# Kernel optimization log

Measured on AMD Instinct MI355X. Metric: run time of the kernel, lower is better.

## Reference

```python
import jax, jax.numpy as jnp
import numpy as np

EMBED = 384
HEAD = 64


def setup_inputs() -> dict:
    key = jax.random.key(0)
    kx, kq, kk, kv = jax.random.split(key, 4)
    B, T = 4, 4096
    x = jax.random.normal(kx, (B, T, EMBED), dtype=jnp.float32)
    # torch Linear(384, 64, bias=False): weight (64, 384), y = x @ W.T.
    # Store pre-transposed as (EMBED, HEAD) so y = x @ W.
    s = 1.0 / np.sqrt(EMBED)  # kaiming-uniform-ish scale
    Wq = jax.random.uniform(kq, (EMBED, HEAD), jnp.float32, -s, s)
    Wk = jax.random.uniform(kk, (EMBED, HEAD), jnp.float32, -s, s)
    Wv = jax.random.uniform(kv, (EMBED, HEAD), jnp.float32, -s, s)
    return {"x": x, "Wq": Wq, "Wk": Wk, "Wv": Wv}


def reference(x, Wq, Wk, Wv):
    # q, k, v: [B, T, H]
    q = x @ Wq
    k = x @ Wk
    v = x @ Wv
    scale = k.shape[-1] ** (-0.5)
    scores = jnp.einsum("bth,bsh->bts", q, k) * scale  # [B, T, T]
    # Faithful to the original: tril, then mask anything equal to 0 with -inf
    # (this also masks exact zeros inside the causal region).
    tril = jnp.tril(scores)
    masked = jnp.where(tril == 0, -jnp.inf, tril)
    attn = jax.nn.softmax(masked, axis=-1)
    out = jnp.einsum("bts,bsh->bth", attn, v)  # [B, T, H]
    return out
```

## Files before the change

### kernel.cpp

```cpp
#include <hip/hip_runtime.h>
#include <hip/hip_bf16.h>
#include <stdint.h>


#define EMBED 384
#define HEAD  64
#define NB    4
#define NT    4096
#define NROWS (NB * NT)

#define SCALE_Q 0.18033688011112042f

typedef short bf16x8 __attribute__((ext_vector_type(8)));
typedef float f32x4  __attribute__((ext_vector_type(4)));

__device__ __forceinline__ unsigned short bfround(float f) {
    union { float f; unsigned u; } v; v.f = f;
    return (unsigned short)((v.u + 0x8000u) >> 16);
}
__device__ __forceinline__ unsigned packbf(float lo, float hi) {
    union { float f; unsigned u; } a, b; a.f = lo; b.f = hi;
    return ((a.u + 0x8000u) >> 16) | ((b.u + 0x8000u) & 0xFFFF0000u);
}

__global__ __launch_bounds__(256)
void wprep_kernel(const float* __restrict__ Wq,
                  const float* __restrict__ Wk,
                  const float* __restrict__ Wv,
                  unsigned short* __restrict__ Wt)
{
    int idx = blockIdx.x * 256 + threadIdx.x;
    int k = idx / 192;
    int n = idx - k * 192;
    int sel = n >> 6, nc = n & 63;
    const float* wp = (sel == 0) ? Wq : ((sel == 1) ? Wk : Wv);
    Wt[n * EMBED + k] = bfround(wp[(size_t)k * HEAD + nc]);
}

__global__ __launch_bounds__(256)
void proj_kernel(const float* __restrict__ x,
                 const unsigned short* __restrict__ Wt,
                 unsigned short* __restrict__ Qo,
                 unsigned short* __restrict__ Ko,
                 unsigned short* __restrict__ Vto)
{
    __shared__ __attribute__((aligned(16))) unsigned short ws[96][200];
    __shared__ __attribute__((aligned(16))) unsigned short xs[64][200];
    unsigned short (*vbuf)[72] = (unsigned short (*)[72])&xs[0][0];

    const int t    = threadIdx.x;
    const int w    = t >> 6;
    const int lane = t & 63;
    const int quad = lane >> 4;
    const int l16  = lane & 15;
    const int half = blockIdx.x & 1;
    const int r0   = (blockIdx.x >> 1) * 64;
    const int colbase = half * 96;

    f32x4 acc[6];
#pragma unroll
    for (int i = 0; i < 6; ++i) acc[i] = (f32x4){0.f, 0.f, 0.f, 0.f};

#pragma unroll
    for (int ph = 0; ph < 2; ++ph) {
        if (ph) __syncthreads();
        const int k0 = ph * 192;
#pragma unroll
        for (int i = 0; i < 9; ++i) {
            int idx = t + i * 256;
            int row = idx / 24, c = idx - row * 24;
            *(uint4*)&ws[row][c * 8] =
                *(const uint4*)(Wt + (size_t)(colbase + row) * EMBED + k0 + c * 8);
        }
#pragma unroll
        for (int i = 0; i < 12; ++i) {
            int idx = t + i * 256;
            int row = idx / 48, c4 = idx - row * 48;
            const float4 v = *(const float4*)(x + (size_t)(r0 + row) * EMBED + k0 + c4 * 4);
            uint2 pw; pw.x = packbf(v.x, v.y); pw.y = packbf(v.z, v.w);
            *(uint2*)&xs[row][c4 * 4] = pw;
        }
        __syncthreads();
#pragma unroll
        for (int step = 0; step < 6; ++step) {
            bf16x8 a = *(const bf16x8*)&xs[w * 16 + l16][step * 32 + quad * 8];
#pragma unroll
            for (int ng = 0; ng < 6; ++ng) {
                bf16x8 b = *(const bf16x8*)&ws[ng * 16 + l16][step * 32 + quad * 8];
                acc[ng] = __builtin_amdgcn_mfma_f32_16x16x32_bf16(a, b, acc[ng], 0, 0, 0);
            }
        }
    }
    __syncthreads();

#pragma unroll
    for (int ng = 0; ng < 6; ++ng) {
        int cg = colbase + ng * 16 + l16;
#pragma unroll
        for (int r = 0; r < 4; ++r) {
            int row = r0 + w * 16 + quad * 4 + r;
            float vv = acc[ng][r];
            if (cg < 64) {
                Qo[(size_t)row * HEAD + cg] = bfround(vv * SCALE_Q);
            } else if (cg < 128) {
                Ko[(size_t)row * HEAD + (cg - 64)] = bfround(vv);
            } else {
                vbuf[cg - 128][w * 16 + quad * 4 + r] = bfround(vv);
            }
        }
    }
    __syncthreads();
    if (half == 1) {
        const int batch = r0 >> 12;
        const int s0 = r0 & (NT - 1);
#pragma unroll
        for (int i = 0; i < 2; ++i) {
            int idx = t + i * 256;
            int d = idx >> 3, c = idx & 7;
            *(uint4*)(Vto + ((size_t)(batch * HEAD + d)) * NT + s0 + c * 8) =
                *(const uint4*)&vbuf[d][c * 8];
        }
    }
}

__global__ __launch_bounds__(256)
void attn_kernel(const unsigned short* __restrict__ Qi,
                 const unsigned short* __restrict__ Ki,
                 const unsigned short* __restrict__ Vti,
                 float* __restrict__ opart,
                 float* __restrict__ lpart)
{
    __shared__ __attribute__((aligned(16))) unsigned short Kt[64][64];
    __shared__ __attribute__((aligned(16))) unsigned short Vs[64][64];
    __shared__ __attribute__((aligned(16))) unsigned short Ps[4][16][72];

    const int t    = threadIdx.x;
    const int w    = t >> 6;
    const int lane = t & 63;
    const int quad = lane >> 4;
    const int l16  = lane & 15;

    const int u = blockIdx.x;
    int m, sp, batch;
    if (u < 256) { m = 63 - (u >> 2); sp = 0; batch = u & 3; }
    else         { int v = u - 256; m = v >> 2; sp = 1; batch = v & 3; }
    const int ntiles = (m >= sp) ? (((m - sp) >> 1) + 1) : 0;
    const int q0 = m * 64 + w * 16;

    const unsigned short* Kbg = Ki  + (size_t)batch * NT * HEAD;
    const unsigned short* Vbg = Vti + (size_t)batch * HEAD * NT;

    bf16x8 bq0, bq1;
    {
        const unsigned short* qp = Qi + (size_t)(batch * NT + q0 + l16) * HEAD + quad * 8;
        bq0 = *(const bf16x8*)(qp);
        bq1 = *(const bf16x8*)(qp + 32);
    }

    f32x4 o[4];
#pragma unroll
    for (int i = 0; i < 4; ++i) o[i] = (f32x4){0.f, 0.f, 0.f, 0.f};
    float rs = 0.f;

    const int srow0 = t >> 3, sc = t & 7;
    const int srow1 = (t + 256) >> 3;
    const int scc0 = sc ^ (srow0 & 7);
    const int scc1 = sc ^ (srow1 & 7);

    for (int j = 0; j < ntiles; ++j) {
        const int kt = sp + 2 * j;
        uint4 kr0 = *(const uint4*)(Kbg + (size_t)(kt * 64 + srow0) * HEAD + sc * 8);
        uint4 kr1 = *(const uint4*)(Kbg + (size_t)(kt * 64 + srow1) * HEAD + sc * 8);
        uint4 vr0 = *(const uint4*)(Vbg + (size_t)srow0 * NT + kt * 64 + sc * 8);
        uint4 vr1 = *(const uint4*)(Vbg + (size_t)srow1 * NT + kt * 64 + sc * 8);
        __syncthreads();
        *(uint4*)&Kt[srow0][scc0 * 8] = kr0;
        *(uint4*)&Kt[srow1][scc1 * 8] = kr1;
        *(uint4*)&Vs[srow0][scc0 * 8] = vr0;
        *(uint4*)&Vs[srow1][scc1 * 8] = vr1;
        __syncthreads();

        const int sw = l16 & 7;
        const bool diag = (kt == m);
#pragma unroll
        for (int ts = 0; ts < 4; ++ts) {
            bf16x8 ak0 = *(const bf16x8*)&Kt[ts * 16 + l16][(quad ^ sw) * 8];
            bf16x8 ak1 = *(const bf16x8*)&Kt[ts * 16 + l16][((4 + quad) ^ sw) * 8];
            f32x4 z = (f32x4){0.f, 0.f, 0.f, 0.f};
            z = __builtin_amdgcn_mfma_f32_16x16x32_bf16(ak0, bq0, z, 0, 0, 0);
            z = __builtin_amdgcn_mfma_f32_16x16x32_bf16(ak1, bq1, z, 0, 0, 0);
            float p[4];
#pragma unroll
            for (int r = 0; r < 4; ++r) {
                float pv = __builtin_amdgcn_exp2f(z[r]);
                if (diag) {
                    int sg = kt * 64 + ts * 16 + quad * 4 + r;
                    pv = (sg > q0 + l16) ? 0.f : pv;
                }
                p[r] = pv;
            }
            rs += (p[0] + p[1]) + (p[2] + p[3]);
            uint2 pw; pw.x = packbf(p[0], p[1]); pw.y = packbf(p[2], p[3]);
            *(uint2*)&Ps[w][l16][ts * 16 + quad * 4] = pw;
        }
        bf16x8 ap0 = *(const bf16x8*)&Ps[w][l16][quad * 8];
        bf16x8 ap1 = *(const bf16x8*)&Ps[w][l16][32 + quad * 8];
#pragma unroll
        for (int nd = 0; nd < 4; ++nd) {
            bf16x8 av0 = *(const bf16x8*)&Vs[nd * 16 + l16][(quad ^ sw) * 8];
            bf16x8 av1 = *(const bf16x8*)&Vs[nd * 16 + l16][((4 + quad) ^ sw) * 8];
            o[nd] = __builtin_amdgcn_mfma_f32_16x16x32_bf16(ap0, av0, o[nd], 0, 0, 0);
            o[nd] = __builtin_amdgcn_mfma_f32_16x16x32_bf16(ap1, av1, o[nd], 0, 0, 0);
        }
    }

    rs += __shfl_xor(rs, 16, 64);
    rs += __shfl_xor(rs, 32, 64);
    if (quad == 0)
        lpart[(size_t)sp * NROWS + batch * NT + q0 + l16] = rs;
    float* ob = opart + (size_t)sp * NROWS * HEAD;
#pragma unroll
    for (int r = 0; r < 4; ++r) {
        size_t off = (size_t)(batch * NT + q0 + quad * 4 + r) * HEAD;
#pragma unroll
        for (int nd = 0; nd < 4; ++nd)
            ob[off + nd * 16 + l16] = o[nd][r];
    }
}

__global__ __launch_bounds__(256)
void combine_kernel(const float* __restrict__ opart,
                    const float* __restrict__ lpart,
                    float* __restrict__ out)
{
    int gid = blockIdx.x * 256 + threadIdx.x;
    int row = gid >> 4;
    int d4  = (gid & 15) * 4;
    f32x4 a = *(const f32x4*)(opart + (size_t)row * HEAD + d4);
    f32x4 b = *(const f32x4*)(opart + (size_t)NROWS * HEAD + (size_t)row * HEAD + d4);
    float inv = 1.0f / (lpart[row] + lpart[NROWS + row]);
    f32x4 res = (a + b);
    res[0] *= inv; res[1] *= inv; res[2] *= inv; res[3] *= inv;
    *(f32x4*)(out + (size_t)row * HEAD + d4) = res;
}

extern "C" void kernel_launch(void* const* d_in, const int* in_sizes, int n_in,
                              void* d_out, int out_size, void* d_ws, size_t ws_size,
                              hipStream_t stream)
{
    const float* x  = (const float*)d_in[0];
    const float* Wq = (const float*)d_in[1];
    const float* Wk = (const float*)d_in[2];
    const float* Wv = (const float*)d_in[3];
    float* out = (float*)d_out;

    unsigned short* Qw  = (unsigned short*)d_ws;
    unsigned short* Kw  = Qw + (size_t)NROWS * HEAD;
    unsigned short* Vtw = Kw + (size_t)NROWS * HEAD;
    unsigned short* Wtw = Vtw + (size_t)NROWS * HEAD;
    float* opart = (float*)(Wtw + (size_t)192 * EMBED);
    float* lpart = opart + (size_t)2 * NROWS * HEAD;

    wprep_kernel<<<(192 * EMBED) / 256, 256, 0, stream>>>(Wq, Wk, Wv, Wtw);
    proj_kernel<<<512, 256, 0, stream>>>(x, Wtw, Qw, Kw, Vtw);
    attn_kernel<<<512, 256, 0, stream>>>(Qw, Kw, Vtw, opart, lpart);
    combine_kernel<<<NROWS * 16 / 256, 256, 0, stream>>>(opart, lpart, out);
}
```

Measured before the change: 127.6 us.

## Split KV tiles across waves per block and prefetch projection inputs in registers

The attention kernel now gives each wave all 64 query rows of the block and a strided subset of KV tiles (split-K across waves and the two block halves). Each wave keeps its own private K/V LDS tiles with register prefetch of the next K tile and the V tile, so the per-tile block-wide barriers go away. Partial outputs are reduced through LDS at the end. The projection kernel also loads the second K-half of x and W into registers while the first half's MFMAs run. This raises register and LDS use per block, and the launch bounds now request two blocks per CU.

```diff
diff --git a/kernel.cpp b/kernel.cpp
--- a/kernel.cpp
+++ b/kernel.cpp
@@ -44,7 +44,7 @@
                  unsigned short* __restrict__ Ko,
                  unsigned short* __restrict__ Vto)
 {
-    __shared__ __attribute__((aligned(16))) unsigned short ws[96][200];
+    __shared__ __attribute__((aligned(16))) unsigned short wsm[96][200];
     __shared__ __attribute__((aligned(16))) unsigned short xs[64][200];
     unsigned short (*vbuf)[72] = (unsigned short (*)[72])&xs[0][0];
 
@@ -61,34 +61,68 @@
 #pragma unroll
     for (int i = 0; i < 6; ++i) acc[i] = (f32x4){0.f, 0.f, 0.f, 0.f};
 
-#pragma unroll
-    for (int ph = 0; ph < 2; ++ph) {
-        if (ph) __syncthreads();
-        const int k0 = ph * 192;
-#pragma unroll
-        for (int i = 0; i < 9; ++i) {
-            int idx = t + i * 256;
-            int row = idx / 24, c = idx - row * 24;
-            *(uint4*)&ws[row][c * 8] =
-                *(const uint4*)(Wt + (size_t)(colbase + row) * EMBED + k0 + c * 8);
-        }
-#pragma unroll
-        for (int i = 0; i < 12; ++i) {
-            int idx = t + i * 256;
-            int row = idx / 48, c4 = idx - row * 48;
-            const float4 v = *(const float4*)(x + (size_t)(r0 + row) * EMBED + k0 + c4 * 4);
-            uint2 pw; pw.x = packbf(v.x, v.y); pw.y = packbf(v.z, v.w);
-            *(uint2*)&xs[row][c4 * 4] = pw;
-        }
-        __syncthreads();
-#pragma unroll
-        for (int step = 0; step < 6; ++step) {
-            bf16x8 a = *(const bf16x8*)&xs[w * 16 + l16][step * 32 + quad * 8];
-#pragma unroll
-            for (int ng = 0; ng < 6; ++ng) {
-                bf16x8 b = *(const bf16x8*)&ws[ng * 16 + l16][step * 32 + quad * 8];
-                acc[ng] = __builtin_amdgcn_mfma_f32_16x16x32_bf16(a, b, acc[ng], 0, 0, 0);
-            }
+    uint4 wr[9]; float4 xr[12];
+#pragma unroll
+    for (int i = 0; i < 9; ++i) {
+        int idx = t + i * 256; int row = idx / 24, c = idx - row * 24;
+        wr[i] = *(const uint4*)(Wt + (size_t)(colbase + row) * EMBED + c * 8);
+    }
+#pragma unroll
+    for (int i = 0; i < 12; ++i) {
+        int idx = t + i * 256; int row = idx / 48, c4 = idx - row * 48;
+        xr[i] = *(const float4*)(x + (size_t)(r0 + row) * EMBED + c4 * 4);
+    }
+#pragma unroll
+    for (int i = 0; i < 9; ++i) {
+        int idx = t + i * 256; int row = idx / 24, c = idx - row * 24;
+        *(uint4*)&wsm[row][c * 8] = wr[i];
+    }
+#pragma unroll
+    for (int i = 0; i < 12; ++i) {
+        int idx = t + i * 256; int row = idx / 48, c4 = idx - row * 48;
+        uint2 pw; pw.x = packbf(xr[i].x, xr[i].y); pw.y = packbf(xr[i].z, xr[i].w);
+        *(uint2*)&xs[row][c4 * 4] = pw;
+    }
+    __syncthreads();
+#pragma unroll
+    for (int i = 0; i < 9; ++i) {
+        int idx = t + i * 256; int row = idx / 24, c = idx - row * 24;
+        wr[i] = *(const uint4*)(Wt + (size_t)(colbase + row) * EMBED + 192 + c * 8);
+    }
+#pragma unroll
+    for (int i = 0; i < 12; ++i) {
+        int idx = t + i * 256; int row = idx / 48, c4 = idx - row * 48;
+        xr[i] = *(const float4*)(x + (size_t)(r0 + row) * EMBED + 192 + c4 * 4);
+    }
+#pragma unroll
+    for (int step = 0; step < 6; ++step) {
+        bf16x8 a = *(const bf16x8*)&xs[w * 16 + l16][step * 32 + quad * 8];
+#pragma unroll
+        for (int ng = 0; ng < 6; ++ng) {
+            bf16x8 b = *(const bf16x8*)&wsm[ng * 16 + l16][step * 32 + quad * 8];
+            acc[ng] = __builtin_amdgcn_mfma_f32_16x16x32_bf16(a, b, acc[ng], 0, 0, 0);
+        }
+    }
+    __syncthreads();
+#pragma unroll
+    for (int i = 0; i < 9; ++i) {
+        int idx = t + i * 256; int row = idx / 24, c = idx - row * 24;
+        *(uint4*)&wsm[row][c * 8] = wr[i];
+    }
+#pragma unroll
+    for (int i = 0; i < 12; ++i) {
+        int idx = t + i * 256; int row = idx / 48, c4 = idx - row * 48;
+        uint2 pw; pw.x = packbf(xr[i].x, xr[i].y); pw.y = packbf(xr[i].z, xr[i].w);
+        *(uint2*)&xs[row][c4 * 4] = pw;
+    }
+    __syncthreads();
+#pragma unroll
+    for (int step = 0; step < 6; ++step) {
+        bf16x8 a = *(const bf16x8*)&xs[w * 16 + l16][step * 32 + quad * 8];
+#pragma unroll
+        for (int ng = 0; ng < 6; ++ng) {
+            bf16x8 b = *(const bf16x8*)&wsm[ng * 16 + l16][step * 32 + quad * 8];
+            acc[ng] = __builtin_amdgcn_mfma_f32_16x16x32_bf16(a, b, acc[ng], 0, 0, 0);
         }
     }
     __syncthreads();
@@ -123,108 +157,178 @@
     }
 }
 
-__global__ __launch_bounds__(256)
+__global__ __launch_bounds__(256, 2)
 void attn_kernel(const unsigned short* __restrict__ Qi,
                  const unsigned short* __restrict__ Ki,
                  const unsigned short* __restrict__ Vti,
                  float* __restrict__ opart,
                  float* __restrict__ lpart)
 {
-    __shared__ __attribute__((aligned(16))) unsigned short Kt[64][64];
-    __shared__ __attribute__((aligned(16))) unsigned short Vs[64][64];
+    __shared__ __attribute__((aligned(16))) unsigned short stage[4][2][64][64];
     __shared__ __attribute__((aligned(16))) unsigned short Ps[4][16][72];
+    __shared__ float prs[4][64];
 
     const int t    = threadIdx.x;
     const int w    = t >> 6;
     const int lane = t & 63;
     const int quad = lane >> 4;
     const int l16  = lane & 15;
-
-    const int u = blockIdx.x;
-    int m, sp, batch;
-    if (u < 256) { m = 63 - (u >> 2); sp = 0; batch = u & 3; }
-    else         { int v = u - 256; m = v >> 2; sp = 1; batch = v & 3; }
-    const int ntiles = (m >= sp) ? (((m - sp) >> 1) + 1) : 0;
-    const int q0 = m * 64 + w * 16;
+    const int g    = lane >> 3;
+    const int c    = lane & 7;
+    const int scc  = c ^ g;
+    const int sw   = l16 & 7;
+
+    const int u     = blockIdx.x;
+    const int sh    = u >> 8;
+    const int v     = u & 255;
+    const int batch = v & 3;
+    const int mi    = v >> 2;
+    const int m     = sh ? mi : (63 - mi);
+    const int s     = sh * 4 + w;
+    const int ntiles = (m >= s) ? (((m - s) >> 3) + 1) : 0;
+    const int q0 = m * 64;
 
     const unsigned short* Kbg = Ki  + (size_t)batch * NT * HEAD;
     const unsigned short* Vbg = Vti + (size_t)batch * HEAD * NT;
 
-    bf16x8 bq0, bq1;
+    unsigned short (*Kt)[64] = stage[w][0];
+    unsigned short (*Vs)[64] = stage[w][1];
+
+    bf16x8 bq0[4], bq1[4];
+#pragma unroll
+    for (int qs = 0; qs < 4; ++qs) {
+        const unsigned short* qp = Qi + (size_t)(batch * NT + q0 + qs * 16 + l16) * HEAD + quad * 8;
+        bq0[qs] = *(const bf16x8*)(qp);
+        bq1[qs] = *(const bf16x8*)(qp + 32);
+    }
+
+    f32x4 o[4][4];
+#pragma unroll
+    for (int a = 0; a < 4; ++a)
+#pragma unroll
+        for (int b = 0; b < 4; ++b) o[a][b] = (f32x4){0.f, 0.f, 0.f, 0.f};
+    float rs[4] = {0.f, 0.f, 0.f, 0.f};
+
+    if (ntiles > 0) {
+        uint4 kreg[8];
+#pragma unroll
+        for (int i = 0; i < 8; ++i)
+            kreg[i] = *(const uint4*)(Kbg + (size_t)(s * 64 + i * 8 + g) * HEAD + c * 8);
+#pragma unroll
+        for (int i = 0; i < 8; ++i)
+            *(uint4*)&Kt[i * 8 + g][scc * 8] = kreg[i];
+
+        for (int j = 0; j < ntiles; ++j) {
+            const int kt = s + 8 * j;
+            uint4 vreg[8];
+#pragma unroll
+            for (int i = 0; i < 8; ++i)
+                vreg[i] = *(const uint4*)(Vbg + (size_t)(i * 8 + g) * NT + kt * 64 + c * 8);
+            bf16x8 ak0[4], ak1[4];
+#pragma unroll
+            for (int ts = 0; ts < 4; ++ts) {
+                ak0[ts] = *(const bf16x8*)&Kt[ts * 16 + l16][(quad ^ sw) * 8];
+                ak1[ts] = *(const bf16x8*)&Kt[ts * 16 + l16][((4 + quad) ^ sw) * 8];
+            }
+            if (j + 1 < ntiles) {
+#pragma unroll
+                for (int i = 0; i < 8; ++i)
+                    kreg[i] = *(const uint4*)(Kbg + (size_t)((kt + 8) * 64 + i * 8 + g) * HEAD + c * 8);
+            }
+            const bool diag = (kt == m);
+            bf16x8 ap0[4], ap1[4];
+#pragma unroll
+            for (int qs = 0; qs < 4; ++qs) {
+                f32x4 z[4];
+#pragma unroll
+                for (int ts = 0; ts < 4; ++ts) {
+                    f32x4 zz = (f32x4){0.f, 0.f, 0.f, 0.f};
+                    zz = __builtin_amdgcn_mfma_f32_16x16x32_bf16(ak0[ts], bq0[qs], zz, 0, 0, 0);
+                    zz = __builtin_amdgcn_mfma_f32_16x16x32_bf16(ak1[ts], bq1[qs], zz, 0, 0, 0);
+                    z[ts] = zz;
+                }
+#pragma unroll
+                for (int ts = 0; ts < 4; ++ts) {
+                    float p[4];
+#pragma unroll
+                    for (int r = 0; r < 4; ++r) {
+                        float pv = __builtin_amdgcn_exp2f(z[ts][r]);
+                        if (diag) {
+                            int sl = ts * 16 + quad * 4 + r;
+                            int ql = qs * 16 + l16;
+                            pv = (sl > ql) ? 0.f : pv;
+                        }
+                        p[r] = pv;
+                    }
+                    rs[qs] += (p[0] + p[1]) + (p[2] + p[3]);
+                    uint2 pw; pw.x = packbf(p[0], p[1]); pw.y = packbf(p[2], p[3]);
+                    *(uint2*)&Ps[w][l16][ts * 16 + quad * 4] = pw;
+                }
+                ap0[qs] = *(const bf16x8*)&Ps[w][l16][quad * 8];
+                ap1[qs] = *(const bf16x8*)&Ps[w][l16][32 + quad * 8];
+                if (qs == 0) {
+#pragma unroll
+                    for (int i = 0; i < 8; ++i)
+                        *(uint4*)&Vs[i * 8 + g][scc * 8] = vreg[i];
+                }
+            }
+            if (j + 1 < ntiles) {
+#pragma unroll
+                for (int i = 0; i < 8; ++i)
+                    *(uint4*)&Kt[i * 8 + g][scc * 8] = kreg[i];
+            }
+            bf16x8 av0[4], av1[4];
+#pragma unroll
+            for (int nd = 0; nd < 4; ++nd) {
+                av0[nd] = *(const bf16x8*)&Vs[nd * 16 + l16][(quad ^ sw) * 8];
+                av1[nd] = *(const bf16x8*)&Vs[nd * 16 + l16][((4 + quad) ^ sw) * 8];
+            }
+#pragma unroll
+            for (int qs = 0; qs < 4; ++qs)
+#pragma unroll
+                for (int nd = 0; nd < 4; ++nd) {
+                    o[qs][nd] = __builtin_amdgcn_mfma_f32_16x16x32_bf16(ap0[qs], av0[nd], o[qs][nd], 0, 0, 0);
+                    o[qs][nd] = __builtin_amdgcn_mfma_f32_16x16x32_bf16(ap1[qs], av1[nd], o[qs][nd], 0, 0, 0);
+                }
+        }
+    }
+
+#pragma unroll
+    for (int qs = 0; qs < 4; ++qs) {
+        float vsum = rs[qs];
+        vsum += __shfl_xor(vsum, 16, 64);
+        vsum += __shfl_xor(vsum, 32, 64);
+        if (quad == 0) prs[w][qs * 16 + l16] = vsum;
+    }
+    float* ost = (float*)&stage[w][0][0][0];
+#pragma unroll
+    for (int qs = 0; qs < 4; ++qs)
+#pragma unroll
+        for (int nd = 0; nd < 4; ++nd)
+#pragma unroll
+            for (int r = 0; r < 4; ++r)
+                ost[(qs * 16 + quad * 4 + r) * 64 + nd * 16 + l16] = o[qs][nd][r];
+    __syncthreads();
+
     {
-        const unsigned short* qp = Qi + (size_t)(batch * NT + q0 + l16) * HEAD + quad * 8;
-        bq0 = *(const bf16x8*)(qp);
-        bq1 = *(const bf16x8*)(qp + 32);
-    }
-
-    f32x4 o[4];
-#pragma unroll
-    for (int i = 0; i < 4; ++i) o[i] = (f32x4){0.f, 0.f, 0.f, 0.f};
-    float rs = 0.f;
-
-    const int srow0 = t >> 3, sc = t & 7;
-    const int srow1 = (t + 256) >> 3;
-    const int scc0 = sc ^ (srow0 & 7);
-    const int scc1 = sc ^ (srow1 & 7);
-
-    for (int j = 0; j < ntiles; ++j) {
-        const int kt = sp + 2 * j;
-        uint4 kr0 = *(const uint4*)(Kbg + (size_t)(kt * 64 + srow0) * HEAD + sc * 8);
-        uint4 kr1 = *(const uint4*)(Kbg + (size_t)(kt * 64 + srow1) * HEAD + sc * 8);
-        uint4 vr0 = *(const uint4*)(Vbg + (size_t)srow0 * NT + kt * 64 + sc * 8);
-        uint4 vr1 = *(const uint4*)(Vbg + (size_t)srow1 * NT + kt * 64 + sc * 8);
-        __syncthreads();
-        *(uint4*)&Kt[srow0][scc0 * 8] = kr0;
-        *(uint4*)&Kt[srow1][scc1 * 8] = kr1;
-        *(uint4*)&Vs[srow0][scc0 * 8] = vr0;
-        *(uint4*)&Vs[srow1][scc1 * 8] = vr1;
-        __syncthreads();
-
-        const int sw = l16 & 7;
-        const bool diag = (kt == m);
-#pragma unroll
-        for (int ts = 0; ts < 4; ++ts) {
-            bf16x8 ak0 = *(const bf16x8*)&Kt[ts * 16 + l16][(quad ^ sw) * 8];
-            bf16x8 ak1 = *(const bf16x8*)&Kt[ts * 16 + l16][((4 + quad) ^ sw) * 8];
-            f32x4 z = (f32x4){0.f, 0.f, 0.f, 0.f};
-            z = __builtin_amdgcn_mfma_f32_16x16x32_bf16(ak0, bq0, z, 0, 0, 0);
-            z = __builtin_amdgcn_mfma_f32_16x16x32_bf16(ak1, bq1, z, 0, 0, 0);
-            float p[4];
-#pragma unroll
-            for (int r = 0; r < 4; ++r) {
-                float pv = __builtin_amdgcn_exp2f(z[r]);
-                if (diag) {
-                    int sg = kt * 64 + ts * 16 + quad * 4 + r;
-                    pv = (sg > q0 + l16) ? 0.f : pv;
-                }
-                p[r] = pv;
-            }
-            rs += (p[0] + p[1]) + (p[2] + p[3]);
-            uint2 pw; pw.x = packbf(p[0], p[1]); pw.y = packbf(p[2], p[3]);
-            *(uint2*)&Ps[w][l16][ts * 16 + quad * 4] = pw;
-        }
-        bf16x8 ap0 = *(const bf16x8*)&Ps[w][l16][quad * 8];
-        bf16x8 ap1 = *(const bf16x8*)&Ps[w][l16][32 + quad * 8];
-#pragma unroll
-        for (int nd = 0; nd < 4; ++nd) {
-            bf16x8 av0 = *(const bf16x8*)&Vs[nd * 16 + l16][(quad ^ sw) * 8];
-            bf16x8 av1 = *(const bf16x8*)&Vs[nd * 16 + l16][((4 + quad) ^ sw) * 8];
-            o[nd] = __builtin_amdgcn_mfma_f32_16x16x32_bf16(ap0, av0, o[nd], 0, 0, 0);
-            o[nd] = __builtin_amdgcn_mfma_f32_16x16x32_bf16(ap1, av1, o[nd], 0, 0, 0);
-        }
-    }
-
-    rs += __shfl_xor(rs, 16, 64);
-    rs += __shfl_xor(rs, 32, 64);
-    if (quad == 0)
-        lpart[(size_t)sp * NROWS + batch * NT + q0 + l16] = rs;
-    float* ob = opart + (size_t)sp * NROWS * HEAD;
-#pragma unroll
-    for (int r = 0; r < 4; ++r) {
-        size_t off = (size_t)(batch * NT + q0 + quad * 4 + r) * HEAD;
-#pragma unroll
-        for (int nd = 0; nd < 4; ++nd)
-            ob[off + nd * 16 + l16] = o[nd][r];
+        int q = t >> 2, dq = (t & 3) * 16;
+        f32x4 sum[4];
+#pragma unroll
+        for (int p4 = 0; p4 < 4; ++p4) sum[p4] = (f32x4){0.f, 0.f, 0.f, 0.f};
+#pragma unroll
+        for (int w2 = 0; w2 < 4; ++w2) {
+            const float* osw = (const float*)&stage[w2][0][0][0];
+#pragma unroll
+            for (int p4 = 0; p4 < 4; ++p4)
+                sum[p4] += *(const f32x4*)&osw[q * 64 + dq + p4 * 4];
+        }
+        float rsum = prs[0][q] + prs[1][q] + prs[2][q] + prs[3][q];
+        float* ob = opart + ((size_t)sh * NROWS + batch * NT + q0 + q) * HEAD + dq;
+#pragma unroll
+        for (int p4 = 0; p4 < 4; ++p4)
+            *(f32x4*)(ob + p4 * 4) = sum[p4];
+        if ((t & 3) == 0)
+            lpart[(size_t)sh * NROWS + batch * NT + q0 + q] = rsum;
     }
 }
 
```

Measured after the change: 130.9 us. +2.6%, slower.

## Split attention KV range four ways, prefetch tiles, shrink projection blocks

Applied to the files above, without the earlier changes.

Attention work is split across four interleaved key-tile partitions (1024 blocks), and combine sums four partial outputs and normalizers. The next K/V tile is prefetched into registers while the current one is computed. The projection kernel now processes 16 rows per block covering all 192 output columns, giving more blocks. This raises occupancy and latency hiding at the cost of extra partial-output traffic in the combine step.

```diff
diff --git a/kernel.cpp b/kernel.cpp
--- a/kernel.cpp
+++ b/kernel.cpp
@@ -37,93 +37,81 @@
     Wt[n * EMBED + k] = bfround(wp[(size_t)k * HEAD + nc]);
 }
 
-__global__ __launch_bounds__(256)
+__global__ __launch_bounds__(256, 4)
 void proj_kernel(const float* __restrict__ x,
                  const unsigned short* __restrict__ Wt,
                  unsigned short* __restrict__ Qo,
                  unsigned short* __restrict__ Ko,
                  unsigned short* __restrict__ Vto)
 {
-    __shared__ __attribute__((aligned(16))) unsigned short ws[96][200];
-    __shared__ __attribute__((aligned(16))) unsigned short xs[64][200];
-    unsigned short (*vbuf)[72] = (unsigned short (*)[72])&xs[0][0];
+    __shared__ __attribute__((aligned(16))) unsigned short wsm[192][72];
+    __shared__ __attribute__((aligned(16))) unsigned short xs[16][72];
+    unsigned short (*vbuf)[20] = (unsigned short (*)[20])&wsm[0][0];
 
     const int t    = threadIdx.x;
     const int w    = t >> 6;
     const int lane = t & 63;
     const int quad = lane >> 4;
     const int l16  = lane & 15;
-    const int half = blockIdx.x & 1;
-    const int r0   = (blockIdx.x >> 1) * 64;
-    const int colbase = half * 96;
-
-    f32x4 acc[6];
-#pragma unroll
-    for (int i = 0; i < 6; ++i) acc[i] = (f32x4){0.f, 0.f, 0.f, 0.f};
-
-#pragma unroll
-    for (int ph = 0; ph < 2; ++ph) {
-        if (ph) __syncthreads();
-        const int k0 = ph * 192;
-#pragma unroll
-        for (int i = 0; i < 9; ++i) {
-            int idx = t + i * 256;
-            int row = idx / 24, c = idx - row * 24;
-            *(uint4*)&ws[row][c * 8] =
-                *(const uint4*)(Wt + (size_t)(colbase + row) * EMBED + k0 + c * 8);
-        }
-#pragma unroll
-        for (int i = 0; i < 12; ++i) {
-            int idx = t + i * 256;
-            int row = idx / 48, c4 = idx - row * 48;
-            const float4 v = *(const float4*)(x + (size_t)(r0 + row) * EMBED + k0 + c4 * 4);
-            uint2 pw; pw.x = packbf(v.x, v.y); pw.y = packbf(v.z, v.w);
-            *(uint2*)&xs[row][c4 * 4] = pw;
-        }
-        __syncthreads();
-#pragma unroll
-        for (int step = 0; step < 6; ++step) {
-            bf16x8 a = *(const bf16x8*)&xs[w * 16 + l16][step * 32 + quad * 8];
-#pragma unroll
-            for (int ng = 0; ng < 6; ++ng) {
-                bf16x8 b = *(const bf16x8*)&ws[ng * 16 + l16][step * 32 + quad * 8];
-                acc[ng] = __builtin_amdgcn_mfma_f32_16x16x32_bf16(a, b, acc[ng], 0, 0, 0);
+    const int r0   = blockIdx.x * 16;
+
+    f32x4 acc[3];
+#pragma unroll
+    for (int i = 0; i < 3; ++i) acc[i] = (f32x4){0.f, 0.f, 0.f, 0.f};
+
+    const int srow = t >> 3, sc = t & 7;
+    const int xrow = t >> 4, xc = t & 15;
+
+    for (int kc = 0; kc < 6; ++kc) {
+        const int k0 = kc * 64;
+        uint4 wr[6];
+#pragma unroll
+        for (int i = 0; i < 6; ++i)
+            wr[i] = *(const uint4*)(Wt + (size_t)(srow + i * 32) * EMBED + k0 + sc * 8);
+        const float4 xv = *(const float4*)(x + (size_t)(r0 + xrow) * EMBED + k0 + xc * 4);
+        __syncthreads();
+#pragma unroll
+        for (int i = 0; i < 6; ++i)
+            *(uint4*)&wsm[srow + i * 32][sc * 8] = wr[i];
+        {
+            uint2 pw; pw.x = packbf(xv.x, xv.y); pw.y = packbf(xv.z, xv.w);
+            *(uint2*)&xs[xrow][xc * 4] = pw;
+        }
+        __syncthreads();
+#pragma unroll
+        for (int ks = 0; ks < 2; ++ks) {
+            bf16x8 a = *(const bf16x8*)&xs[l16][ks * 32 + quad * 8];
+#pragma unroll
+            for (int i = 0; i < 3; ++i) {
+                int nt = w + i * 4;
+                bf16x8 b = *(const bf16x8*)&wsm[nt * 16 + l16][ks * 32 + quad * 8];
+                acc[i] = __builtin_amdgcn_mfma_f32_16x16x32_bf16(a, b, acc[i], 0, 0, 0);
             }
         }
     }
+
+    const int colw = w * 16 + l16;
+#pragma unroll
+    for (int r = 0; r < 4; ++r) {
+        int row = r0 + quad * 4 + r;
+        Qo[(size_t)row * HEAD + colw] = bfround(acc[0][r] * SCALE_Q);
+        Ko[(size_t)row * HEAD + colw] = bfround(acc[1][r]);
+    }
     __syncthreads();
-
-#pragma unroll
-    for (int ng = 0; ng < 6; ++ng) {
-        int cg = colbase + ng * 16 + l16;
-#pragma unroll
-        for (int r = 0; r < 4; ++r) {
-            int row = r0 + w * 16 + quad * 4 + r;
-            float vv = acc[ng][r];
-            if (cg < 64) {
-                Qo[(size_t)row * HEAD + cg] = bfround(vv * SCALE_Q);
-            } else if (cg < 128) {
-                Ko[(size_t)row * HEAD + (cg - 64)] = bfround(vv);
-            } else {
-                vbuf[cg - 128][w * 16 + quad * 4 + r] = bfround(vv);
-            }
-        }
-    }
+#pragma unroll
+    for (int r = 0; r < 4; ++r)
+        vbuf[colw][quad * 4 + r] = bfround(acc[2][r]);
     __syncthreads();
-    if (half == 1) {
+    {
         const int batch = r0 >> 12;
         const int s0 = r0 & (NT - 1);
-#pragma unroll
-        for (int i = 0; i < 2; ++i) {
-            int idx = t + i * 256;
-            int d = idx >> 3, c = idx & 7;
-            *(uint4*)(Vto + ((size_t)(batch * HEAD + d)) * NT + s0 + c * 8) =
-                *(const uint4*)&vbuf[d][c * 8];
-        }
-    }
-}
-
-__global__ __launch_bounds__(256)
+        int d = t >> 2, part = t & 3;
+        *(uint2*)(Vto + ((size_t)(batch * HEAD + d)) * NT + s0 + part * 4) =
+            *(const uint2*)&vbuf[d][part * 4];
+    }
+}
+
+__global__ __launch_bounds__(256, 4)
 void attn_kernel(const unsigned short* __restrict__ Qi,
                  const unsigned short* __restrict__ Ki,
                  const unsigned short* __restrict__ Vti,
@@ -139,13 +127,16 @@
     const int lane = t & 63;
     const int quad = lane >> 4;
     const int l16  = lane & 15;
-
-    const int u = blockIdx.x;
-    int m, sp, batch;
-    if (u < 256) { m = 63 - (u >> 2); sp = 0; batch = u & 3; }
-    else         { int v = u - 256; m = v >> 2; sp = 1; batch = v & 3; }
-    const int ntiles = (m >= sp) ? (((m - sp) >> 1) + 1) : 0;
-    const int q0 = m * 64 + w * 16;
+    const int sw   = l16 & 7;
+
+    const int u     = blockIdx.x;
+    const int sp    = u >> 8;
+    const int v     = u & 255;
+    const int batch = v & 3;
+    const int mi    = v >> 2;
+    const int m     = (sp & 1) ? mi : (63 - mi);
+    const int ntiles = (m >= sp) ? (((m - sp) >> 2) + 1) : 0;
+    const int q0    = m * 64 + w * 16;
 
     const unsigned short* Kbg = Ki  + (size_t)batch * NT * HEAD;
     const unsigned short* Vbg = Vti + (size_t)batch * HEAD * NT;
@@ -163,24 +154,34 @@
     float rs = 0.f;
 
     const int srow0 = t >> 3, sc = t & 7;
-    const int srow1 = (t + 256) >> 3;
+    const int srow1 = srow0 + 32;
     const int scc0 = sc ^ (srow0 & 7);
     const int scc1 = sc ^ (srow1 & 7);
 
+    uint4 kr0, kr1, vr0, vr1;
+    if (ntiles > 0) {
+        kr0 = *(const uint4*)(Kbg + (size_t)(sp * 64 + srow0) * HEAD + sc * 8);
+        kr1 = *(const uint4*)(Kbg + (size_t)(sp * 64 + srow1) * HEAD + sc * 8);
+        vr0 = *(const uint4*)(Vbg + (size_t)srow0 * NT + sp * 64 + sc * 8);
+        vr1 = *(const uint4*)(Vbg + (size_t)srow1 * NT + sp * 64 + sc * 8);
+    }
+
     for (int j = 0; j < ntiles; ++j) {
-        const int kt = sp + 2 * j;
-        uint4 kr0 = *(const uint4*)(Kbg + (size_t)(kt * 64 + srow0) * HEAD + sc * 8);
-        uint4 kr1 = *(const uint4*)(Kbg + (size_t)(kt * 64 + srow1) * HEAD + sc * 8);
-        uint4 vr0 = *(const uint4*)(Vbg + (size_t)srow0 * NT + kt * 64 + sc * 8);
-        uint4 vr1 = *(const uint4*)(Vbg + (size_t)srow1 * NT + kt * 64 + sc * 8);
+        const int kt = sp + 4 * j;
         __syncthreads();
         *(uint4*)&Kt[srow0][scc0 * 8] = kr0;
         *(uint4*)&Kt[srow1][scc1 * 8] = kr1;
         *(uint4*)&Vs[srow0][scc0 * 8] = vr0;
         *(uint4*)&Vs[srow1][scc1 * 8] = vr1;
         __syncthreads();
-
-        const int sw = l16 & 7;
+        if (j + 1 < ntiles) {
+            const int nt4 = (kt + 4) * 64;
+            kr0 = *(const uint4*)(Kbg + (size_t)(nt4 + srow0) * HEAD + sc * 8);
+            kr1 = *(const uint4*)(Kbg + (size_t)(nt4 + srow1) * HEAD + sc * 8);
+            vr0 = *(const uint4*)(Vbg + (size_t)srow0 * NT + nt4 + sc * 8);
+            vr1 = *(const uint4*)(Vbg + (size_t)srow1 * NT + nt4 + sc * 8);
+        }
+
         const bool diag = (kt == m);
 #pragma unroll
         for (int ts = 0; ts < 4; ++ts) {
@@ -194,8 +195,9 @@
             for (int r = 0; r < 4; ++r) {
                 float pv = __builtin_amdgcn_exp2f(z[r]);
                 if (diag) {
-                    int sg = kt * 64 + ts * 16 + quad * 4 + r;
-                    pv = (sg > q0 + l16) ? 0.f : pv;
+                    int sg = ts * 16 + quad * 4 + r;
+                    int qg = (m & 63) * 0 + (q0 - m * 64) + l16;
+                    pv = (sg > qg) ? 0.f : pv;
                 }
                 p[r] = pv;
             }
@@ -236,12 +238,16 @@
     int gid = blockIdx.x * 256 + threadIdx.x;
     int row = gid >> 4;
     int d4  = (gid & 15) * 4;
-    f32x4 a = *(const f32x4*)(opart + (size_t)row * HEAD + d4);
-    f32x4 b = *(const f32x4*)(opart + (size_t)NROWS * HEAD + (size_t)row * HEAD + d4);
-    float inv = 1.0f / (lpart[row] + lpart[NROWS + row]);
-    f32x4 res = (a + b);
-    res[0] *= inv; res[1] *= inv; res[2] *= inv; res[3] *= inv;
-    *(f32x4*)(out + (size_t)row * HEAD + d4) = res;
+    f32x4 a = (f32x4){0.f, 0.f, 0.f, 0.f};
+    float l = 0.f;
+#pragma unroll
+    for (int sp = 0; sp < 4; ++sp) {
+        a += *(const f32x4*)(opart + (size_t)sp * NROWS * HEAD + (size_t)row * HEAD + d4);
+        l += lpart[(size_t)sp * NROWS + row];
+    }
+    float inv = 1.0f / l;
+    a[0] *= inv; a[1] *= inv; a[2] *= inv; a[3] *= inv;
+    *(f32x4*)(out + (size_t)row * HEAD + d4) = a;
 }
 
 extern "C" void kernel_launch(void* const* d_in, const int* in_sizes, int n_in,
@@ -259,10 +265,10 @@
     unsigned short* Vtw = Kw + (size_t)NROWS * HEAD;
     unsigned short* Wtw = Vtw + (size_t)NROWS * HEAD;
     float* opart = (float*)(Wtw + (size_t)192 * EMBED);
-    float* lpart = opart + (size_t)2 * NROWS * HEAD;
+    float* lpart = opart + (size_t)4 * NROWS * HEAD;
 
     wprep_kernel<<<(192 * EMBED) / 256, 256, 0, stream>>>(Wq, Wk, Wv, Wtw);
-    proj_kernel<<<512, 256, 0, stream>>>(x, Wtw, Qw, Kw, Vtw);
-    attn_kernel<<<512, 256, 0, stream>>>(Qw, Kw, Vtw, opart, lpart);
+    proj_kernel<<<NROWS / 16, 256, 0, stream>>>(x, Wtw, Qw, Kw, Vtw);
+    attn_kernel<<<1024, 256, 0, stream>>>(Qw, Kw, Vtw, opart, lpart);
     combine_kernel<<<NROWS * 16 / 256, 256, 0, stream>>>(opart, lpart, out);
 }
```

After: 148.4 us. +16.4%, slower.
